# Kernel optimization log

Measured on AMD Instinct MI355X. Metric: run time of the kernel, lower is better.

The kernel has to match this reference:

```python
import jax, jax.numpy as jnp
from jax import lax
import numpy as np

EPS = 1e-5


def fps(xyz, npoint):
    # farthest point sampling, starts at index 0 (pointnet2 convention). xyz: (B,N,3)
    B, N, _ = xyz.shape
    def step(carry, _):
        dist, last = carry
        lastp = jnp.take_along_axis(xyz, last[:, None, None], axis=1)  # (B,1,3)
        d2 = jnp.sum((xyz - lastp) ** 2, axis=-1)                      # (B,N)
        dist = jnp.minimum(dist, d2)
        nxt = jnp.argmax(dist, axis=-1).astype(jnp.int32)
        return (dist, nxt), last
    init = (jnp.full((B, N), 1e10, xyz.dtype), jnp.zeros((B,), jnp.int32))
    _, idxs = lax.scan(step, init, None, length=npoint)
    return jnp.transpose(idxs)  # (B, npoint)


def gather2(x, idx):
    # x (B,N,C), idx (B,S) -> (B,S,C)
    return jnp.take_along_axis(x, idx[..., None], axis=1)


def gather3(x, idx):
    # x (B,N,C), idx (B,S,K) -> (B,S,K,C)
    return jnp.take_along_axis(x[:, None], idx[..., None], axis=2)


def ball_query(xyz, new_xyz, radius, nsample):
    # first nsample indices (in original point order) within radius; pad with first hit
    d2 = jnp.sum((new_xyz[:, :, None, :] - xyz[:, None, :, :]) ** 2, axis=-1)  # (B,S,N)
    N = xyz.shape[1]
    mask = d2 < radius * radius
    cand = jnp.where(mask, jnp.arange(N, dtype=jnp.int32), N)
    cand = jnp.sort(cand, axis=-1)[..., :nsample]
    first = cand[..., :1]
    cand = jnp.where(cand == N, first, cand)
    return jnp.where(cand == N, 0, cand)


def shared_mlp(h, layers):
    # h: (B,S,K,C); 1x1 conv == per-point linear; BN2d with batch stats; ReLU
    for W, g, b in layers:
        h = jnp.einsum('bskc,cd->bskd', h, W)
        mu = jnp.mean(h, axis=(0, 1, 2))
        var = jnp.var(h, axis=(0, 1, 2))
        h = jax.nn.relu((h - mu) * lax.rsqrt(var + EPS) * g + b)
    return h


def sa_module(xyz, feat, npoint, radius, nsample, layers):
    if npoint is None:  # group-all
        grouped = jnp.concatenate([xyz, feat], axis=-1)[:, None]  # (B,1,N,3+C)
        new_xyz = xyz[:, :1]
    else:
        cidx = fps(xyz, npoint)
        new_xyz = gather2(xyz, cidx)                              # (B,S,3)
        nidx = ball_query(xyz, new_xyz, radius, nsample)          # (B,S,K)
        gxyz = gather3(xyz, nidx) - new_xyz[:, :, None, :]        # centered xyz
        grouped = jnp.concatenate([gxyz, gather3(feat, nidx)], axis=-1)
    return new_xyz, jnp.max(shared_mlp(grouped, layers), axis=2)  # (B,S,D)


def bn1d_relu(x, g, b):
    mu = jnp.mean(x, axis=0)
    var = jnp.var(x, axis=0)
    return jax.nn.relu((x - mu) * lax.rsqrt(var + EPS) * g + b)


def setup_inputs():
    key = jax.random.key(0)
    ks = jax.random.split(key, 16)
    B, NP, NG = 64, 1024, 256
    inp = {}
    # points in a 0.1-side cube so radius-0.02/0.04 balls contain realistic neighbor counts
    inp['pc'] = jax.random.uniform(ks[0], (B, NP, 3), jnp.float32) * 0.1
    inp['gripper_pc'] = jax.random.uniform(ks[1], (B, NG, 3), jnp.float32) * 0.1
    def conv(k, cin, cout):
        return jax.random.normal(k, (cin, cout), jnp.float32) * (1.0 / np.sqrt(cin))
    specs = {'w1a': (7, 64), 'w1b': (64, 64), 'w1c': (64, 128),
             'w2a': (131, 128), 'w2b': (128, 128), 'w2c': (128, 256),
             'w3a': (259, 256), 'w3b': (256, 256), 'w3c': (256, 512)}
    i = 2
    for name, (cin, cout) in specs.items():
        inp[name] = conv(ks[i], cin, cout); i += 1
        inp['g' + name[1:]] = jnp.ones((cout,), jnp.float32)
        inp['b' + name[1:]] = jnp.zeros((cout,), jnp.float32)
    inp['fw1'] = conv(ks[i], 512, 1024); i += 1
    inp['fb1'] = jnp.zeros((1024,), jnp.float32)
    inp['fg1'] = jnp.ones((1024,), jnp.float32)
    inp['fbb1'] = jnp.zeros((1024,), jnp.float32)
    inp['fw2'] = conv(ks[i], 1024, 1024); i += 1
    inp['fb2'] = jnp.zeros((1024,), jnp.float32)
    inp['fg2'] = jnp.ones((1024,), jnp.float32)
    inp['fbb2'] = jnp.zeros((1024,), jnp.float32)
    inp['hw'] = conv(ks[i], 1024, 1); i += 1
    inp['hb'] = jnp.zeros((1,), jnp.float32)
    return inp


def reference(pc, gripper_pc,
              w1a, g1a, b1a, w1b, g1b, b1b, w1c, g1c, b1c,
              w2a, g2a, b2a, w2b, g2b, b2b, w2c, g2c, b2c,
              w3a, g3a, b3a, w3b, g3b, b3b, w3c, g3c, b3c,
              fw1, fb1, fg1, fbb1, fw2, fb2, fg2, fbb2, hw, hb):
    B, NP, _ = pc.shape
    NG = gripper_pc.shape[1]
    xyz = jnp.concatenate([pc, gripper_pc], axis=1)                       # (B,N,3)
    labels = jnp.concatenate([jnp.ones((B, NP, 1), pc.dtype),
                              jnp.zeros((B, NG, 1), pc.dtype)], axis=1)
    feat = jnp.concatenate([xyz, labels], axis=-1)                        # (B,N,4)
    xyz, feat = sa_module(xyz, feat, 128, 0.02, 64,
                          [(w1a, g1a, b1a), (w1b, g1b, b1b), (w1c, g1c, b1c)])
    xyz, feat = sa_module(xyz, feat, 32, 0.04, 128,
                          [(w2a, g2a, b2a), (w2b, g2b, b2b), (w2c, g2c, b2c)])
    _, feat = sa_module(xyz, feat, None, None, None,
                        [(w3a, g3a, b3a), (w3b, g3b, b3b), (w3c, g3c, b3c)])
    x = feat[:, 0]                                                        # (B,512)
    x = bn1d_relu(x @ fw1 + fb1, fg1, fbb1)
    x = bn1d_relu(x @ fw2 + fb2, fg2, fbb2)
    return x @ hw + hb                                                    # (B,1) logits
```

## Files before the change

### kernel.cpp

```cpp
#include <hip/hip_runtime.h>

#define BN_EPS 1e-5f
#define MFMA_B16(a, b, c) __builtin_amdgcn_mfma_f32_16x16x32_bf16((a), (b), (c), 0, 0, 0)

typedef short s16x8 __attribute__((ext_vector_type(8)));
typedef float f32x4v __attribute__((ext_vector_type(4)));

__device__ __forceinline__ unsigned fenc(float f) {
    unsigned u = __float_as_uint(f);
    return (u & 0x80000000u) ? ~u : (u | 0x80000000u);
}
__device__ __forceinline__ float fdec(unsigned e) {
    unsigned u = (e & 0x80000000u) ? (e ^ 0x80000000u) : ~e;
    return __uint_as_float(u);
}
__device__ __forceinline__ unsigned short f2b(float f) {
    unsigned u = __float_as_uint(f);
    unsigned r = u + 0x7FFFu + ((u >> 16) & 1u);
    return (unsigned short)(r >> 16);
}
__device__ __forceinline__ float b2f(unsigned short h) {
    return __uint_as_float(((unsigned)h) << 16);
}

// ... 270 lines not shown
        float rs = rsqrtf(q1[t] * IR - mu * mu + BN_EPS);
        float a = rs * g1[t];
        aA[t] = a; aB[t] = b1[t] - mu * a;
        int n = nidx[(size_t)bs * 64 + t];
        const float* p = xyz + ((size_t)b * 1280 + n) * 3;
        float cx = nx[bs * 3], cy = nx[bs * 3 + 1], cz = nx[bs * 3 + 2];
        float v[7] = { p[0] - cx, p[1] - cy, p[2] - cz, p[0], p[1], p[2], (n < 1024) ? 1.f : 0.f };
        #pragma unroll
        for (int k = 0; k < 7; k++) {
            unsigned short hi = f2b(v[k]);
            Xhi[t * 40 + k] = hi;
            Xlo[t * 40 + k] = f2b(v[k] - b2f(hi));
        }
        for (int k = 7; k < 40; k++) { Xhi[t * 40 + k] = 0; Xlo[t * 40 + k] = 0; }
    }
    __syncthreads();
    int wv = t >> 6, lane = t & 63;
    int quad = lane >> 4, l16 = lane & 15;
    int aoff = quad * 8;

    f32x4v acc[4] = {};
    {
        size_t woff = (size_t)(wv * 16 + l16) * 32 + aoff;
        s16x8 bh = *(const s16x8*)(W1h + woff);
        s16x8 bl = *(const s16x8*)(W1l + woff);
        #pragma unroll
        for (int mt = 0; mt < 4; mt++) {
            s16x8 ah = *(const s16x8*)&Xhi[(mt * 16 + l16) * 40 + aoff];
            s16x8 al = *(const s16x8*)&Xlo[(mt * 16 + l16) * 40 + aoff];
            acc[mt] = MFMA_B16(al, bh, acc[mt]);
            acc[mt] = MFMA_B16(ah, bl, acc[mt]);
            acc[mt] = MFMA_B16(ah, bh, acc[mt]);
        }
    }
    {
        int n = wv * 16 + l16;
        float a = aA[n], bb = aB[n];
        #pragma unroll
        for (int mt = 0; mt < 4; mt++)
            #pragma unroll
            for (int r = 0; r < 4; r++) {
                int m = mt * 16 + quad * 4 + r;
                float h = fmaxf(acc[mt][r] * a + bb, 0.f);
                unsigned short hi = f2b(h);
                Hh[m * 72 + n] = hi;
                Hl[m * 72 + n] = f2b(h - b2f(hi));
            }
    }
    __syncthreads();

    f32x4v ac2[4] = {};
    #pragma unroll
    for (int kc = 0; kc < 64; kc += 32) {
        size_t woff = (size_t)(wv * 16 + l16) * 64 + kc + aoff;
        s16x8 bh = *(const s16x8*)(W2h + woff);
        s16x8 bl = *(const s16x8*)(W2l + woff);
        #pragma unroll
        for (int mt = 0; mt < 4; mt++) {
            s16x8 ah = *(const s16x8*)&Hh[(mt * 16 + l16) * 72 + kc + aoff];
            s16x8 al = *(const s16x8*)&Hl[(mt * 16 + l16) * 72 + kc + aoff];
            ac2[mt] = MFMA_B16(al, bh, ac2[mt]);
            ac2[mt] = MFMA_B16(ah, bl, ac2[mt]);
            ac2[mt] = MFMA_B16(ah, bh, ac2[mt]);
        }
    }
    int n = wv * 16 + l16;
    float s = 0.f, q = 0.f;
    #pragma unroll
    for (int mt = 0; mt < 4; mt++)
        #pragma unroll
        for (int r = 0; r < 4; r++) {
            int m = mt * 16 + quad * 4 + r;
            float v = ac2[mt][r];
            Y[((size_t)bs * 64 + m) * 64 + n] = v;
            s += v; q += v * v;
        }
    s += __shfl_xor(s, 16, 64); q += __shfl_xor(q, 16, 64);
    s += __shfl_xor(s, 32, 64); q += __shfl_xor(q, 32, 64);
    if (quad == 0) { cs[n] = s; cq[n] = q; }
    __syncthreads();
    if (t < 64) { ps[(size_t)bs * 64 + t] = cs[t]; pq[(size_t)bs * 64 + t] = cq[t]; }
}

__global__ __launch_bounds__(256, 4) void sa1_c_kernel(
    const float* __restrict__ Y,
    const unsigned short* __restrict__ Wh, const unsigned short* __restrict__ Wl,
    const float* __restrict__ s2, const float* __restrict__ q2,
    const float* __restrict__ g2, const float* __restrict__ b2,
    float* __restrict__ ps, float* __restrict__ pq,
    float* __restrict__ pmax, float* __restrict__ pmin)
{
    __shared__ unsigned short Xhi[128 * 72], Xlo[128 * 72];
    __shared__ float aA[64], aB[64];
    __shared__ float cs[128], cq[128];
    __shared__ float cmx[2][128], cmn[2][128];
    const float IR = 1.f / 524288.f;
    int bs0 = blockIdx.x * 2;
    size_t rbase = (size_t)blockIdx.x * 128;
    int t = threadIdx.x;
    if (t < 64) {
        float mu = s2[t] * IR;
        float rs = rsqrtf(q2[t] * IR - mu * mu + BN_EPS);
        float a = rs * g2[t];
        aA[t] = a; aB[t] = b2[t] - mu * a;
    }
    __syncthreads();
    {
        int r = t >> 1, seg = t & 1;
        const float4* y4 = (const float4*)(Y + (rbase + r) * 64 + seg * 32);
        float4 v[8];
        #pragma unroll
        for (int i = 0; i < 8; i++) v[i] = y4[i];
        s16x8 ph[4], pl[4];
        #pragma unroll
        for (int i = 0; i < 8; i++) {
            #pragma unroll
            for (int j = 0; j < 4; j++) {
                int e = i * 4 + j;
                int c = seg * 32 + e;
                float x = fmaxf(((const float*)&v[i])[j] * aA[c] + aB[c], 0.f);
                unsigned short hi = f2b(x);
                ph[e >> 3][e & 7] = (short)hi;
                pl[e >> 3][e & 7] = (short)f2b(x - b2f(hi));
            }
        }
        #pragma unroll
        for (int k = 0; k < 4; k++) {
            *(s16x8*)&Xhi[r * 72 + seg * 32 + k * 8] = ph[k];
            *(s16x8*)&Xlo[r * 72 + seg * 32 + k * 8] = pl[k];
        }
    }
    __syncthreads();
    int wv = t >> 6, lane = t & 63;
    int quad = lane >> 4, l16 = lane & 15;
    int aoff = quad * 8;

    f32x4v a3[8][2] = {};
    #pragma unroll
    for (int kc = 0; kc < 64; kc += 32) {
        #pragma unroll
        for (int g = 0; g < 2; g++) {
            s16x8 ah[4], al[4];
            #pragma unroll
            for (int mi = 0; mi < 4; mi++) {
                int mt = g * 4 + mi;
                ah[mi] = *(const s16x8*)&Xhi[(mt * 16 + l16) * 72 + kc + aoff];
                al[mi] = *(const s16x8*)&Xlo[(mt * 16 + l16) * 72 + kc + aoff];
            }
            #pragma unroll
            for (int nt = 0; nt < 2; nt++) {
                size_t woff = (size_t)(wv * 32 + nt * 16 + l16) * 64 + kc + aoff;
                s16x8 bh = *(const s16x8*)(Wh + woff);
                s16x8 bl = *(const s16x8*)(Wl + woff);
                #pragma unroll
                for (int mi = 0; mi < 4; mi++) {
                    int mt = g * 4 + mi;
                    a3[mt][nt] = MFMA_B16(al[mi], bh, a3[mt][nt]);
                    a3[mt][nt] = MFMA_B16(ah[mi], bl, a3[mt][nt]);
                    a3[mt][nt] = MFMA_B16(ah[mi], bh, a3[mt][nt]);
                }
            }
        }
    }
    #pragma unroll
    for (int nt = 0; nt < 2; nt++) {
        int n = wv * 32 + nt * 16 + l16;
        float s = 0.f, q = 0.f;
        float gmx[2], gmn[2];
        #pragma unroll
        for (int g = 0; g < 2; g++) {
            float mx = -3.4e38f, mn_ = 3.4e38f;
            #pragma unroll
            for (int mi = 0; mi < 4; mi++) {
                int mt = g * 4 + mi;
                #pragma unroll
                for (int r = 0; r < 4; r++) {
                    float v = a3[mt][nt][r]; s += v; q += v * v;
                    mx = fmaxf(mx, v); mn_ = fminf(mn_, v);
                }
            }
            gmx[g] = mx; gmn[g] = mn_;
        }
        s += __shfl_xor(s, 16, 64); q += __shfl_xor(q, 16, 64);
        s += __shfl_xor(s, 32, 64); q += __shfl_xor(q, 32, 64);
        #pragma unroll
        for (int g = 0; g < 2; g++) {
            gmx[g] = fmaxf(gmx[g], __shfl_xor(gmx[g], 16, 64));
            gmn[g] = fminf(gmn[g], __shfl_xor(gmn[g], 16, 64));
            gmx[g] = fmaxf(gmx[g], __shfl_xor(gmx[g], 32, 64));
            gmn[g] = fminf(gmn[g], __shfl_xor(gmn[g], 32, 64));
        }
        if (quad == 0) {
            cs[n] = s; cq[n] = q;
            cmx[0][n] = gmx[0]; cmn[0][n] = gmn[0];
            cmx[1][n] = gmx[1]; cmn[1][n] = gmn[1];
        }
    }
    __syncthreads();
    if (t < 128) {
        ps[(size_t)blockIdx.x * 128 + t] = cs[t]; pq[(size_t)blockIdx.x * 128 + t] = cq[t];
        pmax[(size_t)(bs0 + 0) * 128 + t] = cmx[0][t];
        pmin[(size_t)(bs0 + 0) * 128 + t] = cmn[0][t];
        pmax[(size_t)(bs0 + 1) * 128 + t] = cmx[1][t];
        pmin[(size_t)(bs0 + 1) * 128 + t] = cmn[1][t];
    }
}

__global__ __launch_bounds__(256) void bnpool_fin_kernel(
    const float* __restrict__ pmax, const float* __restrict__ pmin,
    const float* __restrict__ sum, const float* __restrict__ sq,
    const float* __restrict__ g, const float* __restrict__ bb,
    float rcnt, float* __restrict__ out, int total, int dmask)
{
    int i = blockIdx.x * 256 + threadIdx.x;
    if (i >= total) return;
    int d = i & dmask;
    float mu = sum[d] * rcnt;
    float rs = rsqrtf(sq[d] * rcnt - mu * mu + BN_EPS);
    float gv = g[d];
    float v = (gv >= 0.f) ? pmax[i] : pmin[i];
    out[i] = fmaxf((v - mu) * rs * gv + bb[d], 0.f);
}

__global__ __launch_bounds__(256, 4) void sa2_a_kernel(
    const float* __restrict__ xyz1, const int* __restrict__ nidx2,
    const float* __restrict__ nx2, const float* __restrict__ feat1,
    const unsigned short* __restrict__ Wh, const unsigned short* __restrict__ Wl,
    float* __restrict__ ps, float* __restrict__ pq, float* __restrict__ Y)
{
    __shared__ unsigned short Xhi[64 * 168], Xlo[64 * 168];
    __shared__ float cs[128], cq[128];
    __shared__ int sn[64];
    int row0 = blockIdx.x * 64;
    int bs = row0 >> 7, b = bs >> 5;
    int t = threadIdx.x;
    if (t < 64) sn[t] = nidx2[(size_t)bs * 128 + (row0 & 127) + t];
    __syncthreads();
    {
        int r = t >> 2, seg = t & 3;
        int n = sn[r];
        size_t base = ((size_t)(b * 128 + n)) * 128 + seg * 32;
        const float4* fr = (const float4*)(feat1 + base);
        float4 v[8];
        #pragma unroll
        for (int i = 0; i < 8; i++) v[i] = fr[i];
        s16x8 ph[4], pl[4];
        #pragma unroll
        for (int i = 0; i < 8; i++) {
            #pragma unroll
            for (int j = 0; j < 4; j++) {
                int e = i * 4 + j;
                float x = ((const float*)&v[i])[j];
                unsigned short hi = f2b(x);
                ph[e >> 3][e & 7] = (short)hi;
                pl[e >> 3][e & 7] = (short)f2b(x - b2f(hi));
            }
        }
        #pragma unroll
        for (int k = 0; k < 4; k++) {
            *(s16x8*)&Xhi[r * 168 + seg * 32 + k * 8] = ph[k];
            *(s16x8*)&Xlo[r * 168 + seg * 32 + k * 8] = pl[k];
        }
        if (seg == 0) {
            float c3x = nx2[bs * 3], c3y = nx2[bs * 3 + 1], c3z = nx2[bs * 3 + 2];
            const float* pz = xyz1 + ((size_t)b * 128 + n) * 3;
            float g3[3] = { pz[0] - c3x, pz[1] - c3y, pz[2] - c3z };
            s16x8 th = {0, 0, 0, 0, 0, 0, 0, 0}, tl = {0, 0, 0, 0, 0, 0, 0, 0};
            #pragma unroll
            for (int i = 0; i < 3; i++) {
                unsigned short hi = f2b(g3[i]);
                th[i] = (short)hi;
                tl[i] = (short)f2b(g3[i] - b2f(hi));
            }
            *(s16x8*)&Xhi[r * 168 + 128] = th;
            *(s16x8*)&Xlo[r * 168 + 128] = tl;
            s16x8 z = {0, 0, 0, 0, 0, 0, 0, 0};
            #pragma unroll
            for (int k = 0; k < 4; k++) {
                *(s16x8*)&Xhi[r * 168 + 136 + k * 8] = z;
                *(s16x8*)&Xlo[r * 168 + 136 + k * 8] = z;
            }
        }
    }
    __syncthreads();
    int wv = t >> 6, lane = t & 63;
    int quad = lane >> 4, l16 = lane & 15;
    int aoff = quad * 8;

    f32x4v acc[4][2] = {};
    #pragma unroll
    for (int kc = 0; kc < 160; kc += 32) {
        s16x8 ah[4], al[4];
        #pragma unroll
        for (int mt = 0; mt < 4; mt++) {
            ah[mt] = *(const s16x8*)&Xhi[(mt * 16 + l16) * 168 + kc + aoff];
            al[mt] = *(const s16x8*)&Xlo[(mt * 16 + l16) * 168 + kc + aoff];
        }
        #pragma unroll
        for (int nt = 0; nt < 2; nt++) {
            size_t woff = (size_t)(wv * 32 + nt * 16 + l16) * 160 + kc + aoff;
            s16x8 bh = *(const s16x8*)(Wh + woff);
            s16x8 bl = *(const s16x8*)(Wl + woff);
            #pragma unroll
            for (int mt = 0; mt < 4; mt++) {
                acc[mt][nt] = MFMA_B16(al[mt], bh, acc[mt][nt]);
                acc[mt][nt] = MFMA_B16(ah[mt], bl, acc[mt][nt]);
                acc[mt][nt] = MFMA_B16(ah[mt], bh, acc[mt][nt]);
            }
        }
    }
    #pragma unroll
    for (int nt = 0; nt < 2; nt++) {
        int n = wv * 32 + nt * 16 + l16;
        float s = 0.f, q = 0.f;
        #pragma unroll
        for (int mt = 0; mt < 4; mt++)
            #pragma unroll
            for (int r = 0; r < 4; r++) {
                int m = mt * 16 + quad * 4 + r;
                float v = acc[mt][nt][r];
                Y[((size_t)row0 + m) * 128 + n] = v;
                s += v; q += v * v;
            }
        s += __shfl_xor(s, 16, 64); q += __shfl_xor(q, 16, 64);
        s += __shfl_xor(s, 32, 64); q += __shfl_xor(q, 32, 64);
        if (quad == 0) { cs[n] = s; cq[n] = q; }
    }
    __syncthreads();
    if (t < 128) { ps[(size_t)blockIdx.x * 128 + t] = cs[t]; pq[(size_t)blockIdx.x * 128 + t] = cq[t]; }
}

__global__ __launch_bounds__(256, 4) void sa2_b_kernel(
    float* __restrict__ Y,
    const unsigned short* __restrict__ Wh, const unsigned short* __restrict__ Wl,
    const float* __restrict__ s1, const float* __restrict__ q1,
    const float* __restrict__ g1, const float* __restrict__ b1,
    float* __restrict__ ps, float* __restrict__ pq)
{
    __shared__ unsigned short Xhi[64 * 136], Xlo[64 * 136];
    __shared__ float aA[128], aB[128];
    __shared__ float cs[128], cq[128];
    const float IR = 1.f / 262144.f;
    int row0 = blockIdx.x * 64;
    int t = threadIdx.x;
    if (t < 128) {
        float mu = s1[t] * IR;
        float rs = rsqrtf(q1[t] * IR - mu * mu + BN_EPS);
        float a = rs * g1[t];
        aA[t] = a; aB[t] = b1[t] - mu * a;
    }
    __syncthreads();
    {
        int r = t >> 2, seg = t & 3;
        const float4* y4 = (const float4*)(Y + ((size_t)row0 + r) * 128 + seg * 32);
        float4 v[8];
        #pragma unroll
        for (int i = 0; i < 8; i++) v[i] = y4[i];
        s16x8 ph[4], pl[4];
        #pragma unroll
        for (int i = 0; i < 8; i++) {
            #pragma unroll
            for (int j = 0; j < 4; j++) {
                int e = i * 4 + j;
                int c = seg * 32 + e;
                float x = fmaxf(((const float*)&v[i])[j] * aA[c] + aB[c], 0.f);
                unsigned short hi = f2b(x);
                ph[e >> 3][e & 7] = (short)hi;
                pl[e >> 3][e & 7] = (short)f2b(x - b2f(hi));
            }
        }
        #pragma unroll
        for (int k = 0; k < 4; k++) {
            *(s16x8*)&Xhi[r * 136 + seg * 32 + k * 8] = ph[k];
            *(s16x8*)&Xlo[r * 136 + seg * 32 + k * 8] = pl[k];
        }
    }
    __syncthreads();
    int wv = t >> 6, lane = t & 63;
    int quad = lane >> 4, l16 = lane & 15;
    int aoff = quad * 8;

    f32x4v ac2[4][2] = {};
    #pragma unroll
    for (int kc = 0; kc < 128; kc += 32) {
        s16x8 ah[4], al[4];
        #pragma unroll
        for (int mt = 0; mt < 4; mt++) {
            ah[mt] = *(const s16x8*)&Xhi[(mt * 16 + l16) * 136 + kc + aoff];
            al[mt] = *(const s16x8*)&Xlo[(mt * 16 + l16) * 136 + kc + aoff];
        }
        #pragma unroll
        for (int nt = 0; nt < 2; nt++) {
            size_t woff = (size_t)(wv * 32 + nt * 16 + l16) * 128 + kc + aoff;
            s16x8 bh = *(const s16x8*)(Wh + woff);
            s16x8 bl = *(const s16x8*)(Wl + woff);
            #pragma unroll
            for (int mt = 0; mt < 4; mt++) {
                ac2[mt][nt] = MFMA_B16(al[mt], bh, ac2[mt][nt]);
                ac2[mt][nt] = MFMA_B16(ah[mt], bl, ac2[mt][nt]);
                ac2[mt][nt] = MFMA_B16(ah[mt], bh, ac2[mt][nt]);
            }
        }
    }
    #pragma unroll
    for (int nt = 0; nt < 2; nt++) {
        int n = wv * 32 + nt * 16 + l16;
        float s = 0.f, q = 0.f;
        #pragma unroll
        for (int mt = 0; mt < 4; mt++)
            #pragma unroll
            for (int r = 0; r < 4; r++) {
                int m = mt * 16 + quad * 4 + r;
                float v = ac2[mt][nt][r];
                Y[((size_t)row0 + m) * 128 + n] = v;
                s += v; q += v * v;
            }
        s += __shfl_xor(s, 16, 64); q += __shfl_xor(q, 16, 64);
        s += __shfl_xor(s, 32, 64); q += __shfl_xor(q, 32, 64);
        if (quad == 0) { cs[n] = s; cq[n] = q; }
    }
    __syncthreads();
    if (t < 128) { ps[(size_t)blockIdx.x * 128 + t] = cs[t]; pq[(size_t)blockIdx.x * 128 + t] = cq[t]; }
}

__global__ __launch_bounds__(256, 4) void sa2_c_kernel(
    const float* __restrict__ Y,
    const unsigned short* __restrict__ Wh, const unsigned short* __restrict__ Wl,
    const float* __restrict__ s2, const float* __restrict__ q2,
    const float* __restrict__ g2, const float* __restrict__ b2,
    float* __restrict__ ps, float* __restrict__ pq,
    unsigned* __restrict__ pmax, unsigned* __restrict__ pmin)
{
    __shared__ unsigned short Xhi[64 * 136], Xlo[64 * 136];
    __shared__ float aA[128], aB[128];
    __shared__ float cs[256], cq[256];
    __shared__ float cmx[256], cmn[256];
    const float IR = 1.f / 262144.f;
    int row0 = blockIdx.x * 64;
    int bs = row0 >> 7;
    int t = threadIdx.x;
    if (t < 128) {
        float mu = s2[t] * IR;
        float rs = rsqrtf(q2[t] * IR - mu * mu + BN_EPS);
        float a = rs * g2[t];
        aA[t] = a; aB[t] = b2[t] - mu * a;
    }
    __syncthreads();
    {
        int r = t >> 2, seg = t & 3;
        const float4* y4 = (const float4*)(Y + ((size_t)row0 + r) * 128 + seg * 32);
        float4 v[8];
        #pragma unroll
        for (int i = 0; i < 8; i++) v[i] = y4[i];
        s16x8 ph[4], pl[4];
        #pragma unroll
        for (int i = 0; i < 8; i++) {
            #pragma unroll
            for (int j = 0; j < 4; j++) {
                int e = i * 4 + j;
                int c = seg * 32 + e;
                float x = fmaxf(((const float*)&v[i])[j] * aA[c] + aB[c], 0.f);
                unsigned short hi = f2b(x);
                ph[e >> 3][e & 7] = (short)hi;
                pl[e >> 3][e & 7] = (short)f2b(x - b2f(hi));
            }
        }
        #pragma unroll
        for (int k = 0; k < 4; k++) {
            *(s16x8*)&Xhi[r * 136 + seg * 32 + k * 8] = ph[k];
            *(s16x8*)&Xlo[r * 136 + seg * 32 + k * 8] = pl[k];
        }
    }
    __syncthreads();
    int wv = t >> 6, lane = t & 63;
    int quad = lane >> 4, l16 = lane & 15;
    int aoff = quad * 8;

    f32x4v a3[4][4] = {};
    #pragma unroll
    for (int kc = 0; kc < 128; kc += 32) {
        s16x8 ah[4], al[4];
        #pragma unroll
        for (int mt = 0; mt < 4; mt++) {
            ah[mt] = *(const s16x8*)&Xhi[(mt * 16 + l16) * 136 + kc + aoff];
            al[mt] = *(const s16x8*)&Xlo[(mt * 16 + l16) * 136 + kc + aoff];
        }
        #pragma unroll
        for (int ct = 0; ct < 4; ct++) {
            size_t woff = (size_t)(wv * 64 + ct * 16 + l16) * 128 + kc + aoff;
            s16x8 bh = *(const s16x8*)(Wh + woff);
            s16x8 bl = *(const s16x8*)(Wl + woff);
            #pragma unroll
            for (int mt = 0; mt < 4; mt++) {
                a3[mt][ct] = MFMA_B16(al[mt], bh, a3[mt][ct]);
                a3[mt][ct] = MFMA_B16(ah[mt], bl, a3[mt][ct]);
                a3[mt][ct] = MFMA_B16(ah[mt], bh, a3[mt][ct]);
            }
        }
    }
    #pragma unroll
    for (int ct = 0; ct < 4; ct++) {
        int n = wv * 64 + ct * 16 + l16;
        float s = 0.f, q = 0.f, mx = -3.4e38f, mn = 3.4e38f;
        #pragma unroll
        for (int mt = 0; mt < 4; mt++)
            #pragma unroll
            for (int r = 0; r < 4; r++) {
                float v = a3[mt][ct][r]; s += v; q += v * v;
                mx = fmaxf(mx, v); mn = fminf(mn, v);
            }
        s += __shfl_xor(s, 16, 64); q += __shfl_xor(q, 16, 64);
        mx = fmaxf(mx, __shfl_xor(mx, 16, 64)); mn = fminf(mn, __shfl_xor(mn, 16, 64));
        s += __shfl_xor(s, 32, 64); q += __shfl_xor(q, 32, 64);
        mx = fmaxf(mx, __shfl_xor(mx, 32, 64)); mn = fminf(mn, __shfl_xor(mn, 32, 64));
        if (quad == 0) { cs[n] = s; cq[n] = q; cmx[n] = mx; cmn[n] = mn; }
    }
    __syncthreads();
    ps[(size_t)blockIdx.x * 256 + t] = cs[t]; pq[(size_t)blockIdx.x * 256 + t] = cq[t];
    atomicMax(&pmax[(size_t)bs * 256 + t], fenc(cmx[t]));
    atomicMin(&pmin[(size_t)bs * 256 + t], fenc(cmn[t]));
}

__global__ __launch_bounds__(256) void grouped3_prep_kernel(
    const float* __restrict__ nx2, const unsigned* __restrict__ pmax,
    const unsigned* __restrict__ pmin, const float* __restrict__ sum,
    const float* __restrict__ sq, const float* __restrict__ g,
    const float* __restrict__ bb, float rcnt, float* __restrict__ out)
{
    int row = blockIdx.x;
    int t = threadIdx.x;
    for (int c = t; c < 259; c += 256) {
        float v;
        if (c < 3) v = nx2[row * 3 + c];
        else {
            int d = c - 3;
            float mu = sum[d] * rcnt;
            float rs = rsqrtf(sq[d] * rcnt - mu * mu + BN_EPS);
            float gv = g[d];
            float x = fdec((gv >= 0.f) ? pmax[(size_t)row * 256 + d] : pmin[(size_t)row * 256 + d]);
            v = fmaxf((x - mu) * rs * gv + bb[d], 0.f);
        }
        out[(size_t)row * 259 + c] = v;
    }
}

__global__ __launch_bounds__(256) void gemm_bn_kernel(
    const float* __restrict__ X, const float* __restrict__ W,
    const float* __restrict__ bias, float* __restrict__ Y,
    const float* __restrict__ isum, const float* __restrict__ isq,
    const float* __restrict__ ig, const float* __restrict__ ib, float ircnt,
    float* __restrict__ osum, float* __restrict__ osq,
    int M, int C, int D)
{
    __shared__ float Xs[64 * 33];
    __shared__ float Ws[32 * 64];
    __shared__ float cs[64], cq[64];
    int m0 = blockIdx.x * 64;
    int d0 = blockIdx.y * 64;
    int t = threadIdx.x;
    int tr = t >> 4, tc = t & 15, r0 = tr * 4, c0 = tc * 4;
    float acc[4][4] = {};
    int nchunk = (C + 31) / 32;
    for (int ch = 0; ch < nchunk; ch++) {
        int kbase = ch * 32;
        for (int f = t; f < 64 * 32; f += 256) {
            int r = f >> 5, c = f & 31; int gc = kbase + c;
            float v = 0.f;
            if (gc < C) {
                v = X[(size_t)(m0 + r) * C + gc];
                if (isum) {
                    float mu = isum[gc] * ircnt;
                    float rs = rsqrtf(isq[gc] * ircnt - mu * mu + BN_EPS);
                    v = fmaxf((v - mu) * rs * ig[gc] + ib[gc], 0.f);
                }
            }
            Xs[r * 33 + c] = v;
        }
        for (int f = t; f < 32 * 64; f += 256) {
            int c = f >> 6, j = f & 63; int gc = kbase + c;
            Ws[f] = (gc < C) ? W[(size_t)gc * D + d0 + j] : 0.f;
        }
        __syncthreads();
        #pragma unroll 8
        for (int kk = 0; kk < 32; kk++) {
            float xv[4], wv[4];
            #pragma unroll
            for (int i = 0; i < 4; i++) xv[i] = Xs[(r0 + i) * 33 + kk];
            #pragma unroll
            for (int j = 0; j < 4; j++) wv[j] = Ws[kk * 64 + c0 + j];
            #pragma unroll
            for (int i = 0; i < 4; i++)
                #pragma unroll
                for (int j = 0; j < 4; j++)
                    acc[i][j] = fmaf(xv[i], wv[j], acc[i][j]);
        }
        __syncthreads();
    }
    if (bias) {
        #pragma unroll
        for (int j = 0; j < 4; j++) {
            float bv = bias[d0 + c0 + j];
            #pragma unroll
            for (int i = 0; i < 4; i++) acc[i][j] += bv;
// ... 147 lines not shown
    const float* w1a = (const float*)d_in[2];  const float* g1a = (const float*)d_in[3];  const float* b1a = (const float*)d_in[4];
    const float* w1b = (const float*)d_in[5];  const float* g1b = (const float*)d_in[6];  const float* b1b = (const float*)d_in[7];
    const float* w1c = (const float*)d_in[8];  const float* g1c = (const float*)d_in[9];  const float* b1c = (const float*)d_in[10];
    const float* w2a = (const float*)d_in[11]; const float* g2a = (const float*)d_in[12]; const float* b2a = (const float*)d_in[13];
    const float* w2b = (const float*)d_in[14]; const float* g2b = (const float*)d_in[15]; const float* b2b = (const float*)d_in[16];
    const float* w2c = (const float*)d_in[17]; const float* g2c = (const float*)d_in[18]; const float* b2c = (const float*)d_in[19];
    const float* w3a = (const float*)d_in[20]; const float* g3a = (const float*)d_in[21]; const float* b3a = (const float*)d_in[22];
    const float* w3b = (const float*)d_in[23]; const float* g3b = (const float*)d_in[24]; const float* b3b = (const float*)d_in[25];
    const float* w3c = (const float*)d_in[26]; const float* g3c = (const float*)d_in[27]; const float* b3c = (const float*)d_in[28];
    const float* fw1 = (const float*)d_in[29]; const float* fb1 = (const float*)d_in[30];
    const float* fg1 = (const float*)d_in[31]; const float* fbb1 = (const float*)d_in[32];
    const float* fw2 = (const float*)d_in[33]; const float* fb2 = (const float*)d_in[34];
    const float* fg2 = (const float*)d_in[35]; const float* fbb2 = (const float*)d_in[36];
    const float* hw  = (const float*)d_in[37]; const float* hb  = (const float*)d_in[38];
    float* out = (float*)d_out;

    char* ws = (char*)d_ws;
    size_t o = 0;
    auto take = [&](size_t nf) { size_t r = o; o += nf * 4; return r; };
    size_t XYZ  = take(245760);
    size_t CID1 = take(8192);
    size_t NID1 = take(524288);
    size_t NX1  = take(24576);
    size_t CID2 = take(2048);
    size_t NID2 = take(262144);
    size_t NX2  = take(6144);
    size_t FE1  = take(1048576);
    size_t GR3  = take(530432);
    size_t H3A  = take(524288);
    size_t H3B  = take(524288);
    size_t H3C  = take(1048576);
    size_t X3   = take(32768);
    size_t Y1   = take(65536);
    size_t Y2   = take(65536);
    size_t P1X  = take(1048576);
    size_t P1N  = take(1048576);
    size_t WT1H = take(10240);
    size_t WT1L = take(10240);
    size_t WT2H = take(8192);
    size_t WT2L = take(8192);
    size_t WT3H = take(16384);
    size_t WT3L = take(16384);
    size_t WA1H = take(1024);
    size_t WA1L = take(1024);
    size_t WB1H = take(2048);
    size_t WB1L = take(2048);
    size_t WC1H = take(4096);
    size_t WC1L = take(4096);
    size_t Z0   = o;
    size_t STT  = take(11 * 2048);
    size_t MOM  = take(64);
    size_t P2X  = take(524288);
    size_t Z1   = o;
    size_t P2N  = take(524288);
    size_t Z2   = o;
    size_t PSB  = take(2097152);
    size_t PQB  = take(2097152);
    size_t YB   = take(33554432);

    #define Fp(x) ((float*)(ws + (x)))
    #define Ip(x) ((int*)(ws + (x)))
    #define Up(x) ((unsigned*)(ws + (x)))
    #define Hp(x) ((unsigned short*)(ws + (x)))
    auto st = [&](int slot) { return Fp(STT + (size_t)slot * 2048 * 4); };

    hipMemsetAsync(ws + Z0, 0, Z1 - Z0, stream);
    hipMemsetAsync(ws + Z1, 0xFF, Z2 - Z1, stream);

    build_xyz_kernel<<<320, 256, 0, stream>>>(pc, gpc, Fp(XYZ));
    prep_w_kernel<<<328, 256, 0, stream>>>(w2a, w2b, w2c, w1a, w1b, w1c,
        Hp(WT1H), Hp(WT1L), Hp(WT2H), Hp(WT2L), Hp(WT3H), Hp(WT3L),
        Hp(WA1H), Hp(WA1L), Hp(WB1H), Hp(WB1L), Hp(WC1H), Hp(WC1L));

    fps_wave_kernel<20><<<64, 64, 0, stream>>>(Fp(XYZ), 1280, 128, Ip(CID1));
    ball_query_kernel<<<dim3(64, 32), 256, 0, stream>>>(Fp(XYZ), Ip(CID1), 1280, 128, 64,
                                                        (float)(0.02 * 0.02), Ip(NID1), Fp(NX1));
    sa1_moment_kernel<<<256, 256, 0, stream>>>(Fp(XYZ), Ip(NID1), Fp(NX1), Fp(MOM));
    sa1_mom_fin_kernel<<<1, 64, 0, stream>>>(Fp(MOM), w1a, st(0), st(0) + 1024);
    sa1_ab_kernel<<<8192, 256, 0, stream>>>(Fp(XYZ), Ip(NID1), Fp(NX1),
        Hp(WA1H), Hp(WA1L), Hp(WB1H), Hp(WB1L),
        st(0), st(0) + 1024, g1a, b1a, Fp(PSB), Fp(PQB), Fp(YB));
    reduce_stats_kernel<<<64, 256, 0, stream>>>(Fp(PSB), Fp(PQB), 8192, 64,
        st(1), st(1) + 1024);
    sa1_c_kernel<<<4096, 256, 0, stream>>>(Fp(YB), Hp(WC1H), Hp(WC1L),
        st(1), st(1) + 1024, g1b, b1b, Fp(PSB), Fp(PQB), Fp(P1X), Fp(P1N));
    reduce_stats_kernel<<<128, 256, 0, stream>>>(Fp(PSB), Fp(PQB), 4096, 128,
        st(2), st(2) + 1024);
    bnpool_fin_kernel<<<4096, 256, 0, stream>>>(Fp(P1X), Fp(P1N), st(2), st(2) + 1024,
                                                g1c, b1c, 1.f / 524288.f, Fp(FE1), 1048576, 127);

    fps_wave_kernel<2><<<64, 64, 0, stream>>>(Fp(NX1), 128, 32, Ip(CID2));
    ball_query_kernel<<<dim3(64, 8), 256, 0, stream>>>(Fp(NX1), Ip(CID2), 128, 32, 128,
                                                       (float)(0.04 * 0.04), Ip(NID2), Fp(NX2));
    sa2_a_kernel<<<4096, 256, 0, stream>>>(Fp(NX1), Ip(NID2), Fp(NX2), Fp(FE1),
        Hp(WT1H), Hp(WT1L), Fp(PSB), Fp(PQB), Fp(YB));
    reduce_stats_kernel<<<128, 256, 0, stream>>>(Fp(PSB), Fp(PQB), 4096, 128,
        st(3), st(3) + 1024);
    sa2_b_kernel<<<4096, 256, 0, stream>>>(Fp(YB), Hp(WT2H), Hp(WT2L),
        st(3), st(3) + 1024, g2a, b2a, Fp(PSB), Fp(PQB));
    reduce_stats_kernel<<<128, 256, 0, stream>>>(Fp(PSB), Fp(PQB), 4096, 128,
        st(4), st(4) + 1024);
    sa2_c_kernel<<<4096, 256, 0, stream>>>(Fp(YB), Hp(WT3H), Hp(WT3L),
        st(4), st(4) + 1024, g2b, b2b, Fp(PSB), Fp(PQB), Up(P2X), Up(P2N));
    reduce_stats_kernel<<<256, 256, 0, stream>>>(Fp(PSB), Fp(PQB), 4096, 256,
        st(5), st(5) + 1024);

    grouped3_prep_kernel<<<2048, 256, 0, stream>>>(Fp(NX2), Up(P2X), Up(P2N),
        st(5), st(5) + 1024, g2c, b2c, 1.f / 262144.f, Fp(GR3));
    gemm_bn_kernel<<<dim3(32, 4), 256, 0, stream>>>(Fp(GR3), w3a, nullptr, Fp(H3A),
        nullptr, nullptr, nullptr, nullptr, 0.f, st(6), st(6) + 1024, 2048, 259, 256);
    gemm_bn_kernel<<<dim3(32, 4), 256, 0, stream>>>(Fp(H3A), w3b, nullptr, Fp(H3B),
        st(6), st(6) + 1024, g3a, b3a, 1.f / 2048.f, st(7), st(7) + 1024, 2048, 256, 256);
    gemm_bn_kernel<<<dim3(32, 8), 256, 0, stream>>>(Fp(H3B), w3c, nullptr, Fp(H3C),
        st(7), st(7) + 1024, g3b, b3b, 1.f / 2048.f, st(8), st(8) + 1024, 2048, 256, 512);
    pool3_kernel<<<128, 256, 0, stream>>>(Fp(H3C), st(8), st(8) + 1024, g3c, b3c, Fp(X3));

    fc_gemm_kernel<<<dim3(16, 16), 256, 0, stream>>>(Fp(X3), fw1,
        nullptr, nullptr, nullptr, nullptr, 0.f, Fp(PSB), 512, 1024);
    fc_fin_kernel<<<256, 256, 0, stream>>>(Fp(PSB), fb1, 1024, 16, Fp(Y1));
    col_stats_kernel<<<4, 256, 0, stream>>>(Fp(Y1), 64, 1024, st(9), st(9) + 1024);
    fc_gemm_kernel<<<dim3(16, 16), 256, 0, stream>>>(Fp(Y1), fw2,
        st(9), st(9) + 1024, fg1, fbb1, 1.f / 64.f, Fp(PSB), 1024, 1024);
    fc_fin_kernel<<<256, 256, 0, stream>>>(Fp(PSB), fb2, 1024, 16, Fp(Y2));
    col_stats_kernel<<<4, 256, 0, stream>>>(Fp(Y2), 64, 1024, st(10), st(10) + 1024);
    head_kernel<<<64, 256, 0, stream>>>(Fp(Y2), st(10), st(10) + 1024, fg2, fbb2, hw, hb, out);

    #undef Fp
    #undef Ip
    #undef Up
    #undef Hp
}
```

Measured before the change: 934.6 us.

## Double threads per block in SA1/SA2 MLP kernels, halve per-wave output tiles

Four MFMA-based shared-MLP kernels now launch 512 threads (8 waves) instead of 256, and each wave computes half as many output tiles. Staging loads are split across more threads. In sa1_c the waves split by row-group and column, and partial sums are combined in shared memory. The aim is more wave-level parallelism and fewer accumulator registers per wave to hide latency, in exchange for more redundant A-fragment LDS reads and weight loads per block.

```diff
diff --git a/kernel.cpp b/kernel.cpp
--- a/kernel.cpp
+++ b/kernel.cpp
@@ -376,7 +376,7 @@
     if (t < 64) { ps[(size_t)bs * 64 + t] = cs[t]; pq[(size_t)bs * 64 + t] = cq[t]; }
 }
 
-__global__ __launch_bounds__(256, 4) void sa1_c_kernel(
+__global__ __launch_bounds__(512, 4) void sa1_c_kernel(
     const float* __restrict__ Y,
     const unsigned short* __restrict__ Wh, const unsigned short* __restrict__ Wl,
     const float* __restrict__ s2, const float* __restrict__ q2,
@@ -386,7 +386,7 @@
 {
     __shared__ unsigned short Xhi[128 * 72], Xlo[128 * 72];
     __shared__ float aA[64], aB[64];
-    __shared__ float cs[128], cq[128];
+    __shared__ float cs2[2][128], cq2[2][128];
     __shared__ float cmx[2][128], cmn[2][128];
     const float IR = 1.f / 524288.f;
     int bs0 = blockIdx.x * 2;
@@ -400,18 +400,18 @@
     }
     __syncthreads();
     {
-        int r = t >> 1, seg = t & 1;
-        const float4* y4 = (const float4*)(Y + (rbase + r) * 64 + seg * 32);
-        float4 v[8];
-        #pragma unroll
-        for (int i = 0; i < 8; i++) v[i] = y4[i];
-        s16x8 ph[4], pl[4];
-        #pragma unroll
-        for (int i = 0; i < 8; i++) {
+        int r = t >> 2, seg = t & 3;
+        const float4* y4 = (const float4*)(Y + (rbase + r) * 64 + seg * 16);
+        float4 v[4];
+        #pragma unroll
+        for (int i = 0; i < 4; i++) v[i] = y4[i];
+        s16x8 ph[2], pl[2];
+        #pragma unroll
+        for (int i = 0; i < 4; i++) {
             #pragma unroll
             for (int j = 0; j < 4; j++) {
                 int e = i * 4 + j;
-                int c = seg * 32 + e;
+                int c = seg * 16 + e;
                 float x = fmaxf(((const float*)&v[i])[j] * aA[c] + aB[c], 0.f);
                 unsigned short hi = f2b(x);
                 ph[e >> 3][e & 7] = (short)hi;
@@ -419,80 +419,64 @@
             }
         }
         #pragma unroll
-        for (int k = 0; k < 4; k++) {
-            *(s16x8*)&Xhi[r * 72 + seg * 32 + k * 8] = ph[k];
-            *(s16x8*)&Xlo[r * 72 + seg * 32 + k * 8] = pl[k];
+        for (int k = 0; k < 2; k++) {
+            *(s16x8*)&Xhi[r * 72 + seg * 16 + k * 8] = ph[k];
+            *(s16x8*)&Xlo[r * 72 + seg * 16 + k * 8] = pl[k];
         }
     }
     __syncthreads();
     int wv = t >> 6, lane = t & 63;
+    int wh = wv >> 2, wc = wv & 3;
     int quad = lane >> 4, l16 = lane & 15;
     int aoff = quad * 8;
 
-    f32x4v a3[8][2] = {};
+    f32x4v a3[4][2] = {};
     #pragma unroll
     for (int kc = 0; kc < 64; kc += 32) {
-        #pragma unroll
-        for (int g = 0; g < 2; g++) {
-            s16x8 ah[4], al[4];
+        s16x8 ah[4], al[4];
+        #pragma unroll
+        for (int mi = 0; mi < 4; mi++) {
+            int mt = wh * 4 + mi;
+            ah[mi] = *(const s16x8*)&Xhi[(mt * 16 + l16) * 72 + kc + aoff];
+            al[mi] = *(const s16x8*)&Xlo[(mt * 16 + l16) * 72 + kc + aoff];
+        }
+        #pragma unroll
+        for (int nt = 0; nt < 2; nt++) {
+            size_t woff = (size_t)(wc * 32 + nt * 16 + l16) * 64 + kc + aoff;
+            s16x8 bh = *(const s16x8*)(Wh + woff);
+            s16x8 bl = *(const s16x8*)(Wl + woff);
             #pragma unroll
             for (int mi = 0; mi < 4; mi++) {
-                int mt = g * 4 + mi;
-                ah[mi] = *(const s16x8*)&Xhi[(mt * 16 + l16) * 72 + kc + aoff];
-                al[mi] = *(const s16x8*)&Xlo[(mt * 16 + l16) * 72 + kc + aoff];
-            }
-            #pragma unroll
-            for (int nt = 0; nt < 2; nt++) {
-                size_t woff = (size_t)(wv * 32 + nt * 16 + l16) * 64 + kc + aoff;
-                s16x8 bh = *(const s16x8*)(Wh + woff);
-                s16x8 bl = *(const s16x8*)(Wl + woff);
-                #pragma unroll
-                for (int mi = 0; mi < 4; mi++) {
-                    int mt = g * 4 + mi;
-                    a3[mt][nt] = MFMA_B16(al[mi], bh, a3[mt][nt]);
-                    a3[mt][nt] = MFMA_B16(ah[mi], bl, a3[mt][nt]);
-                    a3[mt][nt] = MFMA_B16(ah[mi], bh, a3[mt][nt]);
-                }
+                a3[mi][nt] = MFMA_B16(al[mi], bh, a3[mi][nt]);
+                a3[mi][nt] = MFMA_B16(ah[mi], bl, a3[mi][nt]);
+                a3[mi][nt] = MFMA_B16(ah[mi], bh, a3[mi][nt]);
             }
         }
     }
     #pragma unroll
     for (int nt = 0; nt < 2; nt++) {
-        int n = wv * 32 + nt * 16 + l16;
-        float s = 0.f, q = 0.f;
-        float gmx[2], gmn[2];
-        #pragma unroll
-        for (int g = 0; g < 2; g++) {
-            float mx = -3.4e38f, mn_ = 3.4e38f;
-            #pragma unroll
-            for (int mi = 0; mi < 4; mi++) {
-                int mt = g * 4 + mi;
-                #pragma unroll
-                for (int r = 0; r < 4; r++) {
-                    float v = a3[mt][nt][r]; s += v; q += v * v;
-                    mx = fmaxf(mx, v); mn_ = fminf(mn_, v);
-                }
-            }
-            gmx[g] = mx; gmn[g] = mn_;
-        }
+        int n = wc * 32 + nt * 16 + l16;
+        float s = 0.f, q = 0.f, mx = -3.4e38f, mn_ = 3.4e38f;
+        #pragma unroll
+        for (int mi = 0; mi < 4; mi++)
+            #pragma unroll
+            for (int r = 0; r < 4; r++) {
+                float v = a3[mi][nt][r]; s += v; q += v * v;
+                mx = fmaxf(mx, v); mn_ = fminf(mn_, v);
+            }
         s += __shfl_xor(s, 16, 64); q += __shfl_xor(q, 16, 64);
+        mx = fmaxf(mx, __shfl_xor(mx, 16, 64)); mn_ = fminf(mn_, __shfl_xor(mn_, 16, 64));
         s += __shfl_xor(s, 32, 64); q += __shfl_xor(q, 32, 64);
-        #pragma unroll
-        for (int g = 0; g < 2; g++) {
-            gmx[g] = fmaxf(gmx[g], __shfl_xor(gmx[g], 16, 64));
-            gmn[g] = fminf(gmn[g], __shfl_xor(gmn[g], 16, 64));
-            gmx[g] = fmaxf(gmx[g], __shfl_xor(gmx[g], 32, 64));
-            gmn[g] = fminf(gmn[g], __shfl_xor(gmn[g], 32, 64));
-        }
+        mx = fmaxf(mx, __shfl_xor(mx, 32, 64)); mn_ = fminf(mn_, __shfl_xor(mn_, 32, 64));
         if (quad == 0) {
-            cs[n] = s; cq[n] = q;
-            cmx[0][n] = gmx[0]; cmn[0][n] = gmn[0];
-            cmx[1][n] = gmx[1]; cmn[1][n] = gmn[1];
+            cs2[wh][n] = s; cq2[wh][n] = q;
+            cmx[wh][n] = mx; cmn[wh][n] = mn_;
         }
     }
     __syncthreads();
     if (t < 128) {
-        ps[(size_t)blockIdx.x * 128 + t] = cs[t]; pq[(size_t)blockIdx.x * 128 + t] = cq[t];
+        ps[(size_t)blockIdx.x * 128 + t] = cs2[0][t] + cs2[1][t];
+        pq[(size_t)blockIdx.x * 128 + t] = cq2[0][t] + cq2[1][t];
         pmax[(size_t)(bs0 + 0) * 128 + t] = cmx[0][t];
         pmin[(size_t)(bs0 + 0) * 128 + t] = cmn[0][t];
         pmax[(size_t)(bs0 + 1) * 128 + t] = cmx[1][t];
@@ -516,7 +500,7 @@
     out[i] = fmaxf((v - mu) * rs * gv + bb[d], 0.f);
 }
 
-__global__ __launch_bounds__(256, 4) void sa2_a_kernel(
+__global__ __launch_bounds__(512, 4) void sa2_a_kernel(
     const float* __restrict__ xyz1, const int* __restrict__ nidx2,
     const float* __restrict__ nx2, const float* __restrict__ feat1,
     const unsigned short* __restrict__ Wh, const unsigned short* __restrict__ Wl,
@@ -531,16 +515,16 @@
     if (t < 64) sn[t] = nidx2[(size_t)bs * 128 + (row0 & 127) + t];
     __syncthreads();
     {
-        int r = t >> 2, seg = t & 3;
+        int r = t >> 3, seg = t & 7;
         int n = sn[r];
-        size_t base = ((size_t)(b * 128 + n)) * 128 + seg * 32;
+        size_t base = ((size_t)(b * 128 + n)) * 128 + seg * 16;
         const float4* fr = (const float4*)(feat1 + base);
-        float4 v[8];
-        #pragma unroll
-        for (int i = 0; i < 8; i++) v[i] = fr[i];
-        s16x8 ph[4], pl[4];
-        #pragma unroll
-        for (int i = 0; i < 8; i++) {
+        float4 v[4];
+        #pragma unroll
+        for (int i = 0; i < 4; i++) v[i] = fr[i];
+        s16x8 ph[2], pl[2];
+        #pragma unroll
+        for (int i = 0; i < 4; i++) {
             #pragma unroll
             for (int j = 0; j < 4; j++) {
                 int e = i * 4 + j;
@@ -551,9 +535,9 @@
             }
         }
         #pragma unroll
-        for (int k = 0; k < 4; k++) {
-            *(s16x8*)&Xhi[r * 168 + seg * 32 + k * 8] = ph[k];
-            *(s16x8*)&Xlo[r * 168 + seg * 32 + k * 8] = pl[k];
+        for (int k = 0; k < 2; k++) {
+            *(s16x8*)&Xhi[r * 168 + seg * 16 + k * 8] = ph[k];
+            *(s16x8*)&Xlo[r * 168 + seg * 16 + k * 8] = pl[k];
         }
         if (seg == 0) {
             float c3x = nx2[bs * 3], c3y = nx2[bs * 3 + 1], c3z = nx2[bs * 3 + 2];
@@ -581,7 +565,7 @@
     int quad = lane >> 4, l16 = lane & 15;
     int aoff = quad * 8;
 
-    f32x4v acc[4][2] = {};
+    f32x4v acc[4] = {};
     #pragma unroll
     for (int kc = 0; kc < 160; kc += 32) {
         s16x8 ah[4], al[4];
@@ -590,29 +574,25 @@
             ah[mt] = *(const s16x8*)&Xhi[(mt * 16 + l16) * 168 + kc + aoff];
             al[mt] = *(const s16x8*)&Xlo[(mt * 16 + l16) * 168 + kc + aoff];
         }
-        #pragma unroll
-        for (int nt = 0; nt < 2; nt++) {
-            size_t woff = (size_t)(wv * 32 + nt * 16 + l16) * 160 + kc + aoff;
-            s16x8 bh = *(const s16x8*)(Wh + woff);
-            s16x8 bl = *(const s16x8*)(Wl + woff);
-            #pragma unroll
-            for (int mt = 0; mt < 4; mt++) {
-                acc[mt][nt] = MFMA_B16(al[mt], bh, acc[mt][nt]);
-                acc[mt][nt] = MFMA_B16(ah[mt], bl, acc[mt][nt]);
-                acc[mt][nt] = MFMA_B16(ah[mt], bh, acc[mt][nt]);
-            }
-        }
-    }
-    #pragma unroll
-    for (int nt = 0; nt < 2; nt++) {
-        int n = wv * 32 + nt * 16 + l16;
+        size_t woff = (size_t)(wv * 16 + l16) * 160 + kc + aoff;
+        s16x8 bh = *(const s16x8*)(Wh + woff);
+        s16x8 bl = *(const s16x8*)(Wl + woff);
+        #pragma unroll
+        for (int mt = 0; mt < 4; mt++) {
+            acc[mt] = MFMA_B16(al[mt], bh, acc[mt]);
+            acc[mt] = MFMA_B16(ah[mt], bl, acc[mt]);
+            acc[mt] = MFMA_B16(ah[mt], bh, acc[mt]);
+        }
+    }
+    {
+        int n = wv * 16 + l16;
         float s = 0.f, q = 0.f;
         #pragma unroll
         for (int mt = 0; mt < 4; mt++)
             #pragma unroll
             for (int r = 0; r < 4; r++) {
                 int m = mt * 16 + quad * 4 + r;
-                float v = acc[mt][nt][r];
+                float v = acc[mt][r];
                 Y[((size_t)row0 + m) * 128 + n] = v;
                 s += v; q += v * v;
             }
@@ -624,7 +604,7 @@
     if (t < 128) { ps[(size_t)blockIdx.x * 128 + t] = cs[t]; pq[(size_t)blockIdx.x * 128 + t] = cq[t]; }
 }
 
-__global__ __launch_bounds__(256, 4) void sa2_b_kernel(
+__global__ __launch_bounds__(512, 4) void sa2_b_kernel(
     float* __restrict__ Y,
     const unsigned short* __restrict__ Wh, const unsigned short* __restrict__ Wl,
     const float* __restrict__ s1, const float* __restrict__ q1,
@@ -645,18 +625,18 @@
     }
     __syncthreads();
     {
-        int r = t >> 2, seg = t & 3;
-        const float4* y4 = (const float4*)(Y + ((size_t)row0 + r) * 128 + seg * 32);
-        float4 v[8];
-        #pragma unroll
-        for (int i = 0; i < 8; i++) v[i] = y4[i];
-        s16x8 ph[4], pl[4];
-        #pragma unroll
-        for (int i = 0; i < 8; i++) {
+        int r = t >> 3, seg = t & 7;
+        const float4* y4 = (const float4*)(Y + ((size_t)row0 + r) * 128 + seg * 16);
+        float4 v[4];
+        #pragma unroll
+        for (int i = 0; i < 4; i++) v[i] = y4[i];
+        s16x8 ph[2], pl[2];
+        #pragma unroll
+        for (int i = 0; i < 4; i++) {
             #pragma unroll
             for (int j = 0; j < 4; j++) {
                 int e = i * 4 + j;
-                int c = seg * 32 + e;
+                int c = seg * 16 + e;
                 float x = fmaxf(((const float*)&v[i])[j] * aA[c] + aB[c], 0.f);
                 unsigned short hi = f2b(x);
                 ph[e >> 3][e & 7] = (short)hi;
@@ -664,9 +644,9 @@
             }
         }
         #pragma unroll
-        for (int k = 0; k < 4; k++) {
-            *(s16x8*)&Xhi[r * 136 + seg * 32 + k * 8] = ph[k];
-            *(s16x8*)&Xlo[r * 136 + seg * 32 + k * 8] = pl[k];
+        for (int k = 0; k < 2; k++) {
+            *(s16x8*)&Xhi[r * 136 + seg * 16 + k * 8] = ph[k];
+            *(s16x8*)&Xlo[r * 136 + seg * 16 + k * 8] = pl[k];
         }
     }
     __syncthreads();
@@ -674,7 +654,7 @@
     int quad = lane >> 4, l16 = lane & 15;
     int aoff = quad * 8;
 
-    f32x4v ac2[4][2] = {};
+    f32x4v ac2[4] = {};
     #pragma unroll
     for (int kc = 0; kc < 128; kc += 32) {
         s16x8 ah[4], al[4];
@@ -683,29 +663,25 @@
             ah[mt] = *(const s16x8*)&Xhi[(mt * 16 + l16) * 136 + kc + aoff];
             al[mt] = *(const s16x8*)&Xlo[(mt * 16 + l16) * 136 + kc + aoff];
         }
-        #pragma unroll
-        for (int nt = 0; nt < 2; nt++) {
-            size_t woff = (size_t)(wv * 32 + nt * 16 + l16) * 128 + kc + aoff;
-            s16x8 bh = *(const s16x8*)(Wh + woff);
-            s16x8 bl = *(const s16x8*)(Wl + woff);
-            #pragma unroll
-            for (int mt = 0; mt < 4; mt++) {
-                ac2[mt][nt] = MFMA_B16(al[mt], bh, ac2[mt][nt]);
-                ac2[mt][nt] = MFMA_B16(ah[mt], bl, ac2[mt][nt]);
-                ac2[mt][nt] = MFMA_B16(ah[mt], bh, ac2[mt][nt]);
-            }
-        }
-    }
-    #pragma unroll
-    for (int nt = 0; nt < 2; nt++) {
-        int n = wv * 32 + nt * 16 + l16;
+        size_t woff = (size_t)(wv * 16 + l16) * 128 + kc + aoff;
+        s16x8 bh = *(const s16x8*)(Wh + woff);
+        s16x8 bl = *(const s16x8*)(Wl + woff);
+        #pragma unroll
+        for (int mt = 0; mt < 4; mt++) {
+            ac2[mt] = MFMA_B16(al[mt], bh, ac2[mt]);
+            ac2[mt] = MFMA_B16(ah[mt], bl, ac2[mt]);
+            ac2[mt] = MFMA_B16(ah[mt], bh, ac2[mt]);
+        }
+    }
+    {
+        int n = wv * 16 + l16;
         float s = 0.f, q = 0.f;
         #pragma unroll
         for (int mt = 0; mt < 4; mt++)
             #pragma unroll
             for (int r = 0; r < 4; r++) {
                 int m = mt * 16 + quad * 4 + r;
-                float v = ac2[mt][nt][r];
+                float v = ac2[mt][r];
                 Y[((size_t)row0 + m) * 128 + n] = v;
                 s += v; q += v * v;
             }
@@ -717,7 +693,7 @@
     if (t < 128) { ps[(size_t)blockIdx.x * 128 + t] = cs[t]; pq[(size_t)blockIdx.x * 128 + t] = cq[t]; }
 }
 
-__global__ __launch_bounds__(256, 4) void sa2_c_kernel(
+__global__ __launch_bounds__(512, 4) void sa2_c_kernel(
     const float* __restrict__ Y,
     const unsigned short* __restrict__ Wh, const unsigned short* __restrict__ Wl,
     const float* __restrict__ s2, const float* __restrict__ q2,
@@ -741,18 +717,18 @@
     }
     __syncthreads();
     {
-        int r = t >> 2, seg = t & 3;
-        const float4* y4 = (const float4*)(Y + ((size_t)row0 + r) * 128 + seg * 32);
-        float4 v[8];
-        #pragma unroll
-        for (int i = 0; i < 8; i++) v[i] = y4[i];
-        s16x8 ph[4], pl[4];
-        #pragma unroll
-        for (int i = 0; i < 8; i++) {
+        int r = t >> 3, seg = t & 7;
+        const float4* y4 = (const float4*)(Y + ((size_t)row0 + r) * 128 + seg * 16);
+        float4 v[4];
+        #pragma unroll
+        for (int i = 0; i < 4; i++) v[i] = y4[i];
+        s16x8 ph[2], pl[2];
+        #pragma unroll
+        for (int i = 0; i < 4; i++) {
             #pragma unroll
             for (int j = 0; j < 4; j++) {
                 int e = i * 4 + j;
-                int c = seg * 32 + e;
+                int c = seg * 16 + e;
                 float x = fmaxf(((const float*)&v[i])[j] * aA[c] + aB[c], 0.f);
                 unsigned short hi = f2b(x);
                 ph[e >> 3][e & 7] = (short)hi;
@@ -760,9 +736,9 @@
             }
         }
         #pragma unroll
-        for (int k = 0; k < 4; k++) {
-            *(s16x8*)&Xhi[r * 136 + seg * 32 + k * 8] = ph[k];
-            *(s16x8*)&Xlo[r * 136 + seg * 32 + k * 8] = pl[k];
+        for (int k = 0; k < 2; k++) {
+            *(s16x8*)&Xhi[r * 136 + seg * 16 + k * 8] = ph[k];
+            *(s16x8*)&Xlo[r * 136 + seg * 16 + k * 8] = pl[k];
         }
     }
     __syncthreads();
@@ -770,7 +746,7 @@
     int quad = lane >> 4, l16 = lane & 15;
     int aoff = quad * 8;
 
-    f32x4v a3[4][4] = {};
+    f32x4v a3[4][2] = {};
     #pragma unroll
     for (int kc = 0; kc < 128; kc += 32) {
         s16x8 ah[4], al[4];
@@ -780,8 +756,8 @@
             al[mt] = *(const s16x8*)&Xlo[(mt * 16 + l16) * 136 + kc + aoff];
         }
         #pragma unroll
-        for (int ct = 0; ct < 4; ct++) {
-            size_t woff = (size_t)(wv * 64 + ct * 16 + l16) * 128 + kc + aoff;
+        for (int ct = 0; ct < 2; ct++) {
+            size_t woff = (size_t)(wv * 32 + ct * 16 + l16) * 128 + kc + aoff;
             s16x8 bh = *(const s16x8*)(Wh + woff);
             s16x8 bl = *(const s16x8*)(Wl + woff);
             #pragma unroll
@@ -793,8 +769,8 @@
         }
     }
     #pragma unroll
-    for (int ct = 0; ct < 4; ct++) {
-        int n = wv * 64 + ct * 16 + l16;
+    for (int ct = 0; ct < 2; ct++) {
+        int n = wv * 32 + ct * 16 + l16;
         float s = 0.f, q = 0.f, mx = -3.4e38f, mn = 3.4e38f;
         #pragma unroll
         for (int mt = 0; mt < 4; mt++)
@@ -810,9 +786,11 @@
         if (quad == 0) { cs[n] = s; cq[n] = q; cmx[n] = mx; cmn[n] = mn; }
     }
     __syncthreads();
-    ps[(size_t)blockIdx.x * 256 + t] = cs[t]; pq[(size_t)blockIdx.x * 256 + t] = cq[t];
-    atomicMax(&pmax[(size_t)bs * 256 + t], fenc(cmx[t]));
-    atomicMin(&pmin[(size_t)bs * 256 + t], fenc(cmn[t]));
+    if (t < 256) {
+        ps[(size_t)blockIdx.x * 256 + t] = cs[t]; pq[(size_t)blockIdx.x * 256 + t] = cq[t];
+        atomicMax(&pmax[(size_t)bs * 256 + t], fenc(cmx[t]));
+        atomicMin(&pmin[(size_t)bs * 256 + t], fenc(cmn[t]));
+    }
 }
 
 __global__ __launch_bounds__(256) void grouped3_prep_kernel(
@@ -1126,7 +1104,7 @@
         st(0), st(0) + 1024, g1a, b1a, Fp(PSB), Fp(PQB), Fp(YB));
     reduce_stats_kernel<<<64, 256, 0, stream>>>(Fp(PSB), Fp(PQB), 8192, 64,
         st(1), st(1) + 1024);
-    sa1_c_kernel<<<4096, 256, 0, stream>>>(Fp(YB), Hp(WC1H), Hp(WC1L),
+    sa1_c_kernel<<<4096, 512, 0, stream>>>(Fp(YB), Hp(WC1H), Hp(WC1L),
         st(1), st(1) + 1024, g1b, b1b, Fp(PSB), Fp(PQB), Fp(P1X), Fp(P1N));
     reduce_stats_kernel<<<128, 256, 0, stream>>>(Fp(PSB), Fp(PQB), 4096, 128,
         st(2), st(2) + 1024);
@@ -1136,15 +1114,15 @@
     fps_wave_kernel<2><<<64, 64, 0, stream>>>(Fp(NX1), 128, 32, Ip(CID2));
     ball_query_kernel<<<dim3(64, 8), 256, 0, stream>>>(Fp(NX1), Ip(CID2), 128, 32, 128,
                                                        (float)(0.04 * 0.04), Ip(NID2), Fp(NX2));
-    sa2_a_kernel<<<4096, 256, 0, stream>>>(Fp(NX1), Ip(NID2), Fp(NX2), Fp(FE1),
+    sa2_a_kernel<<<4096, 512, 0, stream>>>(Fp(NX1), Ip(NID2), Fp(NX2), Fp(FE1),
         Hp(WT1H), Hp(WT1L), Fp(PSB), Fp(PQB), Fp(YB));
     reduce_stats_kernel<<<128, 256, 0, stream>>>(Fp(PSB), Fp(PQB), 4096, 128,
         st(3), st(3) + 1024);
-    sa2_b_kernel<<<4096, 256, 0, stream>>>(Fp(YB), Hp(WT2H), Hp(WT2L),
+    sa2_b_kernel<<<4096, 512, 0, stream>>>(Fp(YB), Hp(WT2H), Hp(WT2L),
         st(3), st(3) + 1024, g2a, b2a, Fp(PSB), Fp(PQB));
     reduce_stats_kernel<<<128, 256, 0, stream>>>(Fp(PSB), Fp(PQB), 4096, 128,
         st(4), st(4) + 1024);
-    sa2_c_kernel<<<4096, 256, 0, stream>>>(Fp(YB), Hp(WT3H), Hp(WT3L),
+    sa2_c_kernel<<<4096, 512, 0, stream>>>(Fp(YB), Hp(WT3H), Hp(WT3L),
         st(4), st(4) + 1024, g2b, b2b, Fp(PSB), Fp(PQB), Up(P2X), Up(P2N));
     reduce_stats_kernel<<<256, 256, 0, stream>>>(Fp(PSB), Fp(PQB), 4096, 256,
         st(5), st(5) + 1024);
```

Result: faster. 887.4 us (-5.0%).
